# Performance work log

Hardware: AMD Instinct MI355X
Metric: run time of the kernel (lower is better)

Reference implementation:

```python
import jax, jax.numpy as jnp
import numpy as np


def setup_inputs() -> dict:
    key = jax.random.key(0)
    k1, k2 = jax.random.split(key)
    B, T, D, C = 16, 2048, 256, 8
    x = jax.random.normal(k1, (B, T, D), dtype=jnp.float32)
    centers = jax.random.normal(k2, (C, D), dtype=jnp.float32)
    scale = jnp.ones((C,), dtype=jnp.float32)
    return {"x": x, "centers": centers, "scale": scale}


def reference(x, centers, scale):
    # x: (B,T,D), centers: (C,D), scale: (C,)
    # Squared distances ||x - c||^2 via expansion (avoids (B,T,C,D) residual tensor):
    x_sq = jnp.sum(x * x, axis=-1, keepdims=True)          # (B,T,1)
    c_sq = jnp.sum(centers * centers, axis=-1)             # (C,)
    xc = jnp.einsum('btd,cd->btc', x, centers)             # (B,T,C)
    distances = x_sq - 2.0 * xc + c_sq                     # (B,T,C)
    assignment = jax.nn.softmax(-scale * distances, axis=2)  # (B,T,C)
    # sum_t a[b,t,c] * (x[b,t,d] - centers[c,d])
    agg_x = jnp.einsum('btc,btd->bcd', assignment, x)      # (B,C,D)
    a_sum = jnp.sum(assignment, axis=1)                    # (B,C)
    aggregated = agg_x - a_sum[..., None] * centers        # (B,C,D)
    B = x.shape[0]
    return aggregated.reshape(B, -1)
```

## Files before the change

### kernel.cpp

```cpp
#include <hip/hip_runtime.h>
#include <stdint.h>
#include <stddef.h>

#define DD   256
#define CC   8
#define BB   16
#define RPB  64
#define NBLK 512
#define KPB  32
#define XROW 264

#define GLOAD16(g, l) __builtin_amdgcn_global_load_lds(                      \
    (const __attribute__((address_space(1))) void*)(g),                      \
    (__attribute__((address_space(3))) void*)(l), 16, 0, 0)

__device__ __forceinline__ float dot4(float4 a, float4 b) {
  return a.x * b.x + a.y * b.y + a.z * b.z + a.w * b.w;
}

__global__ __launch_bounds__(256) void lde_main(
    const float* __restrict__ x,
    const float* __restrict__ centers,
    const float* __restrict__ scale,
    float* __restrict__ pa,
    float* __restrict__ pas)
{
  __shared__ __align__(16) float x_lds[RPB * XROW];
  __shared__ __align__(16) float c_lds[CC * DD];
  __shared__ __align__(16) float a_lds[RPB * CC];

  const int tid  = threadIdx.x;
  const int lane = tid & 63;
  const int wave = tid >> 6;
  const int blk  = blockIdx.x;

  float sv[CC];
  #pragma unroll
  for (int c = 0; c < CC; ++c) sv[c] = scale[c];

  {
    const int  lrow0 = wave * 16;
    const long grow0 = (long)blk * RPB + lrow0;
    #pragma unroll
    for (int r = 0; r < 16; ++r) {
      const float* g = x + (grow0 + r) * DD + lane * 4;
      GLOAD16(g, &x_lds[(lrow0 + r) * XROW]);
    }
  }
  {
    const float4* cg = (const float4*)centers;
    float4* cl = (float4*)c_lds;
    cl[tid]       = cg[tid];
    cl[tid + 256] = cg[tid + 256];
  }
  asm volatile("s_waitcnt vmcnt(0)" ::: "memory");
  __syncthreads();

  float csqv[CC];
  {
    const int c = lane >> 3, oo = lane & 7;
    float cs = 0.f;
    #pragma unroll
    for (int k = 0; k < 8; ++k) {
      float4 cv = *(const float4*)&c_lds[c * DD + k * 32 + oo * 4];
      cs += dot4(cv, cv);
    }
    cs += __shfl_xor(cs, 1);
    cs += __shfl_xor(cs, 2);
    cs += __shfl_xor(cs, 4);
    #pragma unroll
    for (int cc = 0; cc < CC; ++cc) csqv[cc] = __shfl(cs, cc * 8);
  }

  {
    const int o  = lane & 7;
    const int rl = lane >> 3;
    const int r0 = wave * 16 + rl;
    const float* xr0 = &x_lds[r0 * XROW];
    const float* xr1 = &x_lds[(r0 + 8) * XROW];

    float d0[CC] = {0,0,0,0,0,0,0,0};
    float d1[CC] = {0,0,0,0,0,0,0,0};
    float xq0 = 0.f, xq1 = 0.f;
    #pragma unroll
    for (int k = 0; k < 8; ++k) {
      const float4 xv0 = *(const float4*)&xr0[k * 32 + o * 4];
      const float4 xv1 = *(const float4*)&xr1[k * 32 + o * 4];
      xq0 += dot4(xv0, xv0);
      xq1 += dot4(xv1, xv1);
      #pragma unroll
      for (int c = 0; c < CC; ++c) {
        const float4 cv = *(const float4*)&c_lds[c * DD + k * 32 + o * 4];
        d0[c] += dot4(xv0, cv);
        d1[c] += dot4(xv1, cv);
      }
    }
    xq0 += __shfl_xor(xq0, 1); xq0 += __shfl_xor(xq0, 2); xq0 += __shfl_xor(xq0, 4);
    xq1 += __shfl_xor(xq1, 1); xq1 += __shfl_xor(xq1, 2); xq1 += __shfl_xor(xq1, 4);
    #pragma unroll
    for (int c = 0; c < CC; ++c) {
      d0[c] += __shfl_xor(d0[c], 1); d0[c] += __shfl_xor(d0[c], 2); d0[c] += __shfl_xor(d0[c], 4);
      d1[c] += __shfl_xor(d1[c], 1); d1[c] += __shfl_xor(d1[c], 2); d1[c] += __shfl_xor(d1[c], 4);
    }

    {
      float lgt[CC], m = -1e30f;
      #pragma unroll
      for (int c = 0; c < CC; ++c) { lgt[c] = -sv[c] * (xq0 - 2.f * d0[c] + csqv[c]); m = fmaxf(m, lgt[c]); }
      float e[CC], ssum = 0.f;
      #pragma unroll
      for (int c = 0; c < CC; ++c) { e[c] = __expf(lgt[c] - m); ssum += e[c]; }
      const float inv = 1.f / ssum;
      float eo = (o == 0) ? e[0] : (o == 1) ? e[1] : (o == 2) ? e[2] : (o == 3) ? e[3]
               : (o == 4) ? e[4] : (o == 5) ? e[5] : (o == 6) ? e[6] : e[7];
      a_lds[r0 * CC + o] = eo * inv;
    }
    {
      float lgt[CC], m = -1e30f;
      #pragma unroll
      for (int c = 0; c < CC; ++c) { lgt[c] = -sv[c] * (xq1 - 2.f * d1[c] + csqv[c]); m = fmaxf(m, lgt[c]); }
      float e[CC], ssum = 0.f;
      #pragma unroll
      for (int c = 0; c < CC; ++c) { e[c] = __expf(lgt[c] - m); ssum += e[c]; }
      const float inv = 1.f / ssum;
      float eo = (o == 0) ? e[0] : (o == 1) ? e[1] : (o == 2) ? e[2] : (o == 3) ? e[3]
               : (o == 4) ? e[4] : (o == 5) ? e[5] : (o == 6) ? e[6] : e[7];
      a_lds[(r0 + 8) * CC + o] = eo * inv;
    }
  }
  __syncthreads();

  if (wave == 0) {
    const int c = lane >> 3, oo = lane & 7;
    float s = 0.f;
    #pragma unroll
    for (int j = 0; j < 8; ++j) s += a_lds[(j * 8 + oo) * CC + c];
    s += __shfl_xor(s, 1);
    s += __shfl_xor(s, 2);
    s += __shfl_xor(s, 4);
    if (oo == 0) pas[c * NBLK + blk] = s;
  }

  float4 acc[CC];
  #pragma unroll
  for (int c = 0; c < CC; ++c) acc[c] = make_float4(0.f, 0.f, 0.f, 0.f);
  {
    const float2 av = *(const float2*)&a_lds[(wave * 16 + (lane >> 2)) * CC + (lane & 3) * 2];
    #pragma unroll
    for (int r = 0; r < 16; ++r) {
      const float4 xv = *(const float4*)&x_lds[(wave * 16 + r) * XROW + lane * 4];
      #pragma unroll
      for (int c = 0; c < CC; ++c) {
        const float a = __shfl((c & 1) ? av.y : av.x, r * 4 + (c >> 1));
        acc[c].x += a * xv.x; acc[c].y += a * xv.y; acc[c].z += a * xv.z; acc[c].w += a * xv.w;
      }
    }
  }
  __syncthreads();

  float* p_lds = x_lds;
  #pragma unroll
  for (int c = 0; c < CC; ++c)
    *(float4*)&p_lds[(wave * CC + c) * DD + lane * 4] = acc[c];
  __syncthreads();
  {
    const int c = tid >> 5;
    const int g = tid & 31;
    #pragma unroll
    for (int h = 0; h < 2; ++h) {
      const int d4 = g + 32 * h;
      float4 s0 = *(const float4*)&p_lds[(0 * CC + c) * DD + d4 * 4];
      float4 s1 = *(const float4*)&p_lds[(1 * CC + c) * DD + d4 * 4];
      float4 s2 = *(const float4*)&p_lds[(2 * CC + c) * DD + d4 * 4];
      float4 s3 = *(const float4*)&p_lds[(3 * CC + c) * DD + d4 * 4];
      float4 s = make_float4(s0.x + s1.x + s2.x + s3.x, s0.y + s1.y + s2.y + s3.y,
                             s0.z + s1.z + s2.z + s3.z, s0.w + s1.w + s2.w + s3.w);
      *(float4*)&pa[((size_t)c * NBLK + blk) * DD + d4 * 4] = s;
    }
  }
}

__global__ __launch_bounds__(256) void lde_finalize(
    const float* __restrict__ pa,
    const float* __restrict__ pas,
    const float* __restrict__ centers,
    float* __restrict__ out)
{
  __shared__ __align__(16) float r_lds[4][DD];
  const int b  = blockIdx.x >> 3;
  const int c  = blockIdx.x & 7;
  const int kq = threadIdx.x >> 6;
  const int d4 = threadIdx.x & 63;

  const float* base = pa + ((size_t)c * NBLK + b * KPB) * DD;
  float4 s = make_float4(0.f, 0.f, 0.f, 0.f);
  #pragma unroll
  for (int j = 0; j < 8; ++j) {
    const float4 v = *(const float4*)&base[(kq * 8 + j) * DD + d4 * 4];
    s.x += v.x; s.y += v.y; s.z += v.z; s.w += v.w;
  }
  *(float4*)&r_lds[kq][d4 * 4] = s;
  __syncthreads();

  if (kq == 0) {
    float4 t0 = *(const float4*)&r_lds[0][d4 * 4];
    float4 t1 = *(const float4*)&r_lds[1][d4 * 4];
    float4 t2 = *(const float4*)&r_lds[2][d4 * 4];
    float4 t3 = *(const float4*)&r_lds[3][d4 * 4];
    float4 t = make_float4(t0.x + t1.x + t2.x + t3.x, t0.y + t1.y + t2.y + t3.y,
                           t0.z + t1.z + t2.z + t3.z, t0.w + t1.w + t2.w + t3.w);
    float v = pas[c * NBLK + b * KPB + (d4 & 31)];
    v += __shfl_xor(v, 1); v += __shfl_xor(v, 2); v += __shfl_xor(v, 4);
    v += __shfl_xor(v, 8); v += __shfl_xor(v, 16);
    const float4 cv = *(const float4*)&centers[c * DD + d4 * 4];
    float4 o4 = make_float4(t.x - v * cv.x, t.y - v * cv.y, t.z - v * cv.z, t.w - v * cv.w);
    *(float4*)&out[(size_t)(b * CC + c) * DD + d4 * 4] = o4;
  }
}

extern "C" void kernel_launch(void* const* d_in, const int* in_sizes, int n_in,
                              void* d_out, int out_size, void* d_ws, size_t ws_size,
                              hipStream_t stream)
{
  const float* x       = (const float*)d_in[0];
  const float* centers = (const float*)d_in[1];
  const float* scale   = (const float*)d_in[2];
  float* out = (float*)d_out;

  float* pa  = (float*)d_ws;
  float* pas = pa + (size_t)CC * NBLK * DD;

  lde_main<<<NBLK, 256, 0, stream>>>(x, centers, scale, pa, pas);
  lde_finalize<<<BB * CC, 256, 0, stream>>>(pa, pas, centers, out);
}
```

Measured before the change: 85.98 us.

## Overlap x tile arrival with compute via split vmcnt waits per half-tile

Each wave now processes its 16 rows as two halves. It waits only for the first 8 asynchronous global-to-LDS row loads (vmcnt(8)) before computing distances, softmax and the weighted accumulation for those rows, while the second half is still in flight. The centers load is issued into registers before the x loads and stored to LDS afterwards, and the block barrier now waits only on LDS counters. The aggregation reads assignment weights as float4 broadcasts from LDS instead of using per-element cross-lane shuffles. The design relies on each wave reading only its own x rows and on the hand-written vmcnt counts matching the number of outstanding loads, which makes it fragile.

Result: slower. 89.66 us (+4.3%).

```diff
diff --git a/kernel.cpp b/kernel.cpp
--- a/kernel.cpp
+++ b/kernel.cpp
@@ -34,27 +34,27 @@
   const int wave = tid >> 6;
   const int blk  = blockIdx.x;
 
+  const float4 cg0 = ((const float4*)centers)[tid];
+  const float4 cg1 = ((const float4*)centers)[tid + 256];
+  __builtin_amdgcn_sched_barrier(0);
+
+  const int  lrow0 = wave * 16;
+  const long grow0 = (long)blk * RPB + lrow0;
+  #pragma unroll
+  for (int r = 0; r < 16; ++r)
+    GLOAD16(x + (grow0 + r) * DD + lane * 4, &x_lds[(lrow0 + r) * XROW]);
+  __builtin_amdgcn_sched_barrier(0);
+
+  ((float4*)c_lds)[tid]       = cg0;
+  ((float4*)c_lds)[tid + 256] = cg1;
+
   float sv[CC];
   #pragma unroll
   for (int c = 0; c < CC; ++c) sv[c] = scale[c];
 
-  {
-    const int  lrow0 = wave * 16;
-    const long grow0 = (long)blk * RPB + lrow0;
-    #pragma unroll
-    for (int r = 0; r < 16; ++r) {
-      const float* g = x + (grow0 + r) * DD + lane * 4;
-      GLOAD16(g, &x_lds[(lrow0 + r) * XROW]);
-    }
-  }
-  {
-    const float4* cg = (const float4*)centers;
-    float4* cl = (float4*)c_lds;
-    cl[tid]       = cg[tid];
-    cl[tid + 256] = cg[tid + 256];
-  }
-  asm volatile("s_waitcnt vmcnt(0)" ::: "memory");
-  __syncthreads();
+  asm volatile("s_waitcnt lgkmcnt(0)" ::: "memory");
+  __builtin_amdgcn_s_barrier();
+  __builtin_amdgcn_sched_barrier(0);
 
   float csqv[CC];
   {
@@ -62,7 +62,7 @@
     float cs = 0.f;
     #pragma unroll
     for (int k = 0; k < 8; ++k) {
-      float4 cv = *(const float4*)&c_lds[c * DD + k * 32 + oo * 4];
+      const float4 cv = *(const float4*)&c_lds[c * DD + k * 32 + oo * 4];
       cs += dot4(cv, cv);
     }
     cs += __shfl_xor(cs, 1);
@@ -72,62 +72,78 @@
     for (int cc = 0; cc < CC; ++cc) csqv[cc] = __shfl(cs, cc * 8);
   }
 
-  {
-    const int o  = lane & 7;
-    const int rl = lane >> 3;
-    const int r0 = wave * 16 + rl;
-    const float* xr0 = &x_lds[r0 * XROW];
-    const float* xr1 = &x_lds[(r0 + 8) * XROW];
-
-    float d0[CC] = {0,0,0,0,0,0,0,0};
-    float d1[CC] = {0,0,0,0,0,0,0,0};
-    float xq0 = 0.f, xq1 = 0.f;
-    #pragma unroll
-    for (int k = 0; k < 8; ++k) {
-      const float4 xv0 = *(const float4*)&xr0[k * 32 + o * 4];
-      const float4 xv1 = *(const float4*)&xr1[k * 32 + o * 4];
-      xq0 += dot4(xv0, xv0);
-      xq1 += dot4(xv1, xv1);
+  const int o  = lane & 7;
+  const int rl = lane >> 3;
+  float4 acc[CC];
+  #pragma unroll
+  for (int c = 0; c < CC; ++c) acc[c] = make_float4(0.f, 0.f, 0.f, 0.f);
+
+  #pragma unroll
+  for (int h = 0; h < 2; ++h) {
+    if (h == 0) { asm volatile("s_waitcnt vmcnt(8)" ::: "memory"); }
+    else        { asm volatile("s_waitcnt vmcnt(0)" ::: "memory"); }
+    __builtin_amdgcn_sched_barrier(0);
+
+    {
+      const int  row = lrow0 + h * 8 + rl;
+      const float* xr = &x_lds[row * XROW];
+      float dots[CC] = {0,0,0,0,0,0,0,0};
+      float xsq = 0.f;
+      #pragma unroll
+      for (int k = 0; k < 8; ++k) {
+        const float4 xv = *(const float4*)&xr[k * 32 + o * 4];
+        xsq += dot4(xv, xv);
+        #pragma unroll
+        for (int c = 0; c < CC; ++c) {
+          const float4 cv = *(const float4*)&c_lds[c * DD + k * 32 + o * 4];
+          dots[c] += dot4(xv, cv);
+        }
+      }
+      xsq += __shfl_xor(xsq, 1); xsq += __shfl_xor(xsq, 2); xsq += __shfl_xor(xsq, 4);
       #pragma unroll
       for (int c = 0; c < CC; ++c) {
-        const float4 cv = *(const float4*)&c_lds[c * DD + k * 32 + o * 4];
-        d0[c] += dot4(xv0, cv);
-        d1[c] += dot4(xv1, cv);
+        dots[c] += __shfl_xor(dots[c], 1);
+        dots[c] += __shfl_xor(dots[c], 2);
+        dots[c] += __shfl_xor(dots[c], 4);
       }
-    }
-    xq0 += __shfl_xor(xq0, 1); xq0 += __shfl_xor(xq0, 2); xq0 += __shfl_xor(xq0, 4);
-    xq1 += __shfl_xor(xq1, 1); xq1 += __shfl_xor(xq1, 2); xq1 += __shfl_xor(xq1, 4);
-    #pragma unroll
-    for (int c = 0; c < CC; ++c) {
-      d0[c] += __shfl_xor(d0[c], 1); d0[c] += __shfl_xor(d0[c], 2); d0[c] += __shfl_xor(d0[c], 4);
-      d1[c] += __shfl_xor(d1[c], 1); d1[c] += __shfl_xor(d1[c], 2); d1[c] += __shfl_xor(d1[c], 4);
-    }
-
-    {
       float lgt[CC], m = -1e30f;
       #pragma unroll
-      for (int c = 0; c < CC; ++c) { lgt[c] = -sv[c] * (xq0 - 2.f * d0[c] + csqv[c]); m = fmaxf(m, lgt[c]); }
+      for (int c = 0; c < CC; ++c) {
+        lgt[c] = -sv[c] * (xsq - 2.f * dots[c] + csqv[c]);
+        m = fmaxf(m, lgt[c]);
+      }
       float e[CC], ssum = 0.f;
       #pragma unroll
       for (int c = 0; c < CC; ++c) { e[c] = __expf(lgt[c] - m); ssum += e[c]; }
       const float inv = 1.f / ssum;
-      float eo = (o == 0) ? e[0] : (o == 1) ? e[1] : (o == 2) ? e[2] : (o == 3) ? e[3]
-               : (o == 4) ? e[4] : (o == 5) ? e[5] : (o == 6) ? e[6] : e[7];
-      a_lds[r0 * CC + o] = eo * inv;
-    }
-    {
-      float lgt[CC], m = -1e30f;
-      #pragma unroll
-      for (int c = 0; c < CC; ++c) { lgt[c] = -sv[c] * (xq1 - 2.f * d1[c] + csqv[c]); m = fmaxf(m, lgt[c]); }
-      float e[CC], ssum = 0.f;
-      #pragma unroll
-      for (int c = 0; c < CC; ++c) { e[c] = __expf(lgt[c] - m); ssum += e[c]; }
-      const float inv = 1.f / ssum;
-      float eo = (o == 0) ? e[0] : (o == 1) ? e[1] : (o == 2) ? e[2] : (o == 3) ? e[3]
-               : (o == 4) ? e[4] : (o == 5) ? e[5] : (o == 6) ? e[6] : e[7];
-      a_lds[(r0 + 8) * CC + o] = eo * inv;
-    }
-  }
+      const float eo = (o == 0) ? e[0] : (o == 1) ? e[1] : (o == 2) ? e[2] : (o == 3) ? e[3]
+                     : (o == 4) ? e[4] : (o == 5) ? e[5] : (o == 6) ? e[6] : e[7];
+      a_lds[row * CC + o] = eo * inv;
+    }
+
+    #pragma unroll
+    for (int r = 0; r < 8; ++r) {
+      const int  row = lrow0 + h * 8 + r;
+      const float4 xv = *(const float4*)&x_lds[row * XROW + lane * 4];
+      const float4 a0 = *(const float4*)&a_lds[row * CC];
+      const float4 a1 = *(const float4*)&a_lds[row * CC + 4];
+      acc[0].x += a0.x * xv.x; acc[0].y += a0.x * xv.y; acc[0].z += a0.x * xv.z; acc[0].w += a0.x * xv.w;
+      acc[1].x += a0.y * xv.x; acc[1].y += a0.y * xv.y; acc[1].z += a0.y * xv.z; acc[1].w += a0.y * xv.w;
+      acc[2].x += a0.z * xv.x; acc[2].y += a0.z * xv.y; acc[2].z += a0.z * xv.z; acc[2].w += a0.z * xv.w;
+      acc[3].x += a0.w * xv.x; acc[3].y += a0.w * xv.y; acc[3].z += a0.w * xv.z; acc[3].w += a0.w * xv.w;
+      acc[4].x += a1.x * xv.x; acc[4].y += a1.x * xv.y; acc[4].z += a1.x * xv.z; acc[4].w += a1.x * xv.w;
+      acc[5].x += a1.y * xv.x; acc[5].y += a1.y * xv.y; acc[5].z += a1.y * xv.z; acc[5].w += a1.y * xv.w;
+      acc[6].x += a1.z * xv.x; acc[6].y += a1.z * xv.y; acc[6].z += a1.z * xv.z; acc[6].w += a1.z * xv.w;
+      acc[7].x += a1.w * xv.x; acc[7].y += a1.w * xv.y; acc[7].z += a1.w * xv.z; acc[7].w += a1.w * xv.w;
+    }
+  }
+
+  __syncthreads();
+
+  float* p_lds = x_lds;
+  #pragma unroll
+  for (int c = 0; c < CC; ++c)
+    *(float4*)&p_lds[(wave * CC + c) * DD + lane * 4] = acc[c];
   __syncthreads();
 
   if (wave == 0) {
@@ -141,40 +157,18 @@
     if (oo == 0) pas[c * NBLK + blk] = s;
   }
 
-  float4 acc[CC];
-  #pragma unroll
-  for (int c = 0; c < CC; ++c) acc[c] = make_float4(0.f, 0.f, 0.f, 0.f);
-  {
-    const float2 av = *(const float2*)&a_lds[(wave * 16 + (lane >> 2)) * CC + (lane & 3) * 2];
-    #pragma unroll
-    for (int r = 0; r < 16; ++r) {
-      const float4 xv = *(const float4*)&x_lds[(wave * 16 + r) * XROW + lane * 4];
-      #pragma unroll
-      for (int c = 0; c < CC; ++c) {
-        const float a = __shfl((c & 1) ? av.y : av.x, r * 4 + (c >> 1));
-        acc[c].x += a * xv.x; acc[c].y += a * xv.y; acc[c].z += a * xv.z; acc[c].w += a * xv.w;
-      }
-    }
-  }
-  __syncthreads();
-
-  float* p_lds = x_lds;
-  #pragma unroll
-  for (int c = 0; c < CC; ++c)
-    *(float4*)&p_lds[(wave * CC + c) * DD + lane * 4] = acc[c];
-  __syncthreads();
   {
     const int c = tid >> 5;
     const int g = tid & 31;
     #pragma unroll
-    for (int h = 0; h < 2; ++h) {
-      const int d4 = g + 32 * h;
-      float4 s0 = *(const float4*)&p_lds[(0 * CC + c) * DD + d4 * 4];
-      float4 s1 = *(const float4*)&p_lds[(1 * CC + c) * DD + d4 * 4];
-      float4 s2 = *(const float4*)&p_lds[(2 * CC + c) * DD + d4 * 4];
-      float4 s3 = *(const float4*)&p_lds[(3 * CC + c) * DD + d4 * 4];
-      float4 s = make_float4(s0.x + s1.x + s2.x + s3.x, s0.y + s1.y + s2.y + s3.y,
-                             s0.z + s1.z + s2.z + s3.z, s0.w + s1.w + s2.w + s3.w);
+    for (int hh = 0; hh < 2; ++hh) {
+      const int d4 = g + 32 * hh;
+      const float4 s0 = *(const float4*)&p_lds[(0 * CC + c) * DD + d4 * 4];
+      const float4 s1 = *(const float4*)&p_lds[(1 * CC + c) * DD + d4 * 4];
+      const float4 s2 = *(const float4*)&p_lds[(2 * CC + c) * DD + d4 * 4];
+      const float4 s3 = *(const float4*)&p_lds[(3 * CC + c) * DD + d4 * 4];
+      const float4 s = make_float4(s0.x + s1.x + s2.x + s3.x, s0.y + s1.y + s2.y + s3.y,
+                                   s0.z + s1.z + s2.z + s3.z, s0.w + s1.w + s2.w + s3.w);
       *(float4*)&pa[((size_t)c * NBLK + blk) * DD + d4 * 4] = s;
     }
   }
@@ -203,18 +197,18 @@
   __syncthreads();
 
   if (kq == 0) {
-    float4 t0 = *(const float4*)&r_lds[0][d4 * 4];
-    float4 t1 = *(const float4*)&r_lds[1][d4 * 4];
-    float4 t2 = *(const float4*)&r_lds[2][d4 * 4];
-    float4 t3 = *(const float4*)&r_lds[3][d4 * 4];
-    float4 t = make_float4(t0.x + t1.x + t2.x + t3.x, t0.y + t1.y + t2.y + t3.y,
-                           t0.z + t1.z + t2.z + t3.z, t0.w + t1.w + t2.w + t3.w);
+    const float4 t0 = *(const float4*)&r_lds[0][d4 * 4];
+    const float4 t1 = *(const float4*)&r_lds[1][d4 * 4];
+    const float4 t2 = *(const float4*)&r_lds[2][d4 * 4];
+    const float4 t3 = *(const float4*)&r_lds[3][d4 * 4];
+    const float4 t = make_float4(t0.x + t1.x + t2.x + t3.x, t0.y + t1.y + t2.y + t3.y,
+                                 t0.z + t1.z + t2.z + t3.z, t0.w + t1.w + t2.w + t3.w);
     float v = pas[c * NBLK + b * KPB + (d4 & 31)];
     v += __shfl_xor(v, 1); v += __shfl_xor(v, 2); v += __shfl_xor(v, 4);
     v += __shfl_xor(v, 8); v += __shfl_xor(v, 16);
     const float4 cv = *(const float4*)&centers[c * DD + d4 * 4];
-    float4 o4 = make_float4(t.x - v * cv.x, t.y - v * cv.y, t.z - v * cv.z, t.w - v * cv.w);
-    *(float4*)&out[(size_t)(b * CC + c) * DD + d4 * 4] = o4;
+    *(float4*)&out[(size_t)(b * CC + c) * DD + d4 * 4] =
+        make_float4(t.x - v * cv.x, t.y - v * cv.y, t.z - v * cv.z, t.w - v * cv.w);
   }
 }
 
```
